# Optimization experiments

Measured on AMD Instinct MI355X. Metric: run time of the kernel, lower is better.

## Reference

```python
import jax, jax.numpy as jnp
import numpy as np

B, N, C_IN, C_CH = 1, 512, 128, 128

def layer_norm(x, g, b, eps=1e-5):
    mu = jnp.mean(x, axis=-1, keepdims=True)
    var = jnp.var(x, axis=-1, keepdims=True)
    return (x - mu) * jax.lax.rsqrt(var + eps) * g + b

def setup_inputs() -> dict:
    key = jax.random.key(0)
    ks = jax.random.split(key, 16)
    s = 0.02
    # weights stored as [in, out] (torch Linear uses y = x @ W.T + b; we pre-transpose)
    return {
        "z": jax.random.normal(ks[0], (B, N, N, C_IN), jnp.float32),
        "mask": jax.random.randint(ks[1], (B, N, N), 0, 2).astype(bool),
        "g_in": jnp.ones((C_IN,), jnp.float32),
        "b_in": jnp.zeros((C_IN,), jnp.float32),
        "Wa": jax.random.normal(ks[2], (C_IN, C_CH), jnp.float32) * s,
        "ba": jnp.zeros((C_CH,), jnp.float32),
        "Wga": jax.random.normal(ks[3], (C_IN, C_CH), jnp.float32) * s,
        "bga": jax.random.normal(ks[4], (C_CH,), jnp.float32) * s,
        "Wb": jax.random.normal(ks[5], (C_IN, C_CH), jnp.float32) * s,
        "bb": jnp.zeros((C_CH,), jnp.float32),
        "Wgb": jax.random.normal(ks[6], (C_IN, C_CH), jnp.float32) * s,
        "bgb": jax.random.normal(ks[7], (C_CH,), jnp.float32) * s,
        "g_o": jnp.ones((C_CH,), jnp.float32),
        "b_o": jnp.zeros((C_CH,), jnp.float32),
        "Wgo": jax.random.normal(ks[8], (C_IN, C_IN), jnp.float32) * s,
        "bgo": jax.random.normal(ks[9], (C_IN,), jnp.float32) * s,
        "Wo": jax.random.normal(ks[10], (C_CH, C_IN), jnp.float32) * s,
        "bo": jnp.zeros((C_IN,), jnp.float32),
    }

def reference(z, mask, g_in, b_in, Wa, ba, Wga, bga, Wb, bb, Wgb, bgb,
              g_o, b_o, Wgo, bgo, Wo, bo):
    zn = layer_norm(z, g_in, b_in)                                  # [B,N,N,Cin]
    a = jax.nn.sigmoid(zn @ Wga + bga) * (zn @ Wa + ba)             # [B,N,N,Cch]
    b = jax.nn.sigmoid(zn @ Wgb + bgb) * (zn @ Wb + bb)
    m = mask[..., None]                                             # [B,N,N,1]
    a = jnp.where(m, 0.0, a)
    b = jnp.where(m, 0.0, b)
    # axis == 1: k[b,i,j,o] = sum_k a[b,i,k,o] * b[b,j,k,o]
    k = jnp.einsum('biko,bjko->bijo', a, b)
    return jax.nn.sigmoid(zn @ Wgo + bgo) * (layer_norm(k, g_o, b_o) @ Wo + bo)
```

## Files before the change

### kernel.cpp

```cpp
#include <hip/hip_runtime.h>

#define NDIM 512
#define CDIM 128
#define RDIM (NDIM * NDIM)

typedef __attribute__((ext_vector_type(8))) short bf16x8;
typedef __attribute__((ext_vector_type(8))) unsigned short ushort8;
typedef __attribute__((ext_vector_type(4))) float f32x4;

__device__ __forceinline__ float bf2f(unsigned short u) {
  union { unsigned int i; float f; } v; v.i = ((unsigned int)u) << 16; return v.f;
}
__device__ __forceinline__ unsigned short f2bf(float f) {
  union { float f; unsigned int i; } v; v.f = f;
  unsigned int r = v.i + 0x7fffu + ((v.i >> 16) & 1u);
  return (unsigned short)(r >> 16);
}
__device__ __forceinline__ float sigm(float x) { return 1.0f / (1.0f + __expf(-x)); }

__device__ __forceinline__ int sw(int row, int col) {
  return (row << 7) + ((((col >> 3) ^ (row & 7)) << 3) | (col & 7));
}

__global__ __launch_bounds__(256) void k0_prep(
    const float* __restrict__ Wga, const float* __restrict__ Wa,
    const float* __restrict__ Wgb, const float* __restrict__ Wb,
    const float* __restrict__ Wgo, const float* __restrict__ Wo,
    unsigned short* __restrict__ wsW) {
  __shared__ unsigned short T[128 * 130];
  const float* src;
  switch (blockIdx.x) {
    case 0: src = Wga; break;
    case 1: src = Wa;  break;
    case 2: src = Wgb; break;
    case 3: src = Wb;  break;
    case 4: src = Wgo; break;
    default: src = Wo; break;
  }
  unsigned short* dst = wsW + blockIdx.x * (CDIM * CDIM);
  const int t = threadIdx.x;
  const int r = t >> 1, hf = t & 1;
  const float* s = src + r * CDIM + hf * 64;
  for (int i = 0; i < 64; i++) T[r * 130 + hf * 64 + i] = f2bf(s[i]);
  __syncthreads();
  unsigned short* d = dst + r * CDIM + hf * 64;
  for (int i = 0; i < 64; i++) d[i] = T[(hf * 64 + i) * 130 + r];
}

__global__ __launch_bounds__(256) void k1_proj(
    const float* __restrict__ z, const int* __restrict__ mask,
    const float* __restrict__ g_in, const float* __restrict__ b_in,
    const float* __restrict__ bga, const float* __restrict__ ba,
    const float* __restrict__ bgb, const float* __restrict__ bb,
    const float* __restrict__ bgo, const unsigned short* __restrict__ wsW,
    unsigned short* __restrict__ a_t, unsigned short* __restrict__ b_t,
    float* __restrict__ gate_out) {
  __shared__ unsigned short Xs[CDIM * CDIM];
  __shared__ unsigned short WT[CDIM * CDIM];
  const int t = threadIdx.x;
  const int lane = t & 63;
  const int w = t >> 6;
  const int l15 = lane & 15;
  const int lq = lane >> 4;
  const int row0 = blockIdx.x * 128;

  {
    const int row = t >> 1, hf = t & 1;
    const float4* zp = (const float4*)(z + (size_t)(row0 + row) * CDIM + hf * 64);
    float4 v[16];
    float s = 0.f, s2 = 0.f;
#pragma unroll
    for (int i = 0; i < 16; i++) {
      float4 x = zp[i];
      v[i] = x;
      s += x.x + x.y + x.z + x.w;
      s2 += x.x * x.x + x.y * x.y + x.z * x.z + x.w * x.w;
    }
    s += __shfl_xor(s, 1);
    s2 += __shfl_xor(s2, 1);
    const float mean = s * 0.0078125f;
    const float var = s2 * 0.0078125f - mean * mean;
    const float rs = rsqrtf(var + 1e-5f);
    const float4* gp = (const float4*)(g_in + hf * 64);
    const float4* bp = (const float4*)(b_in + hf * 64);
#pragma unroll
    for (int u = 0; u < 8; u++) {
      float4 x0 = v[2 * u], x1 = v[2 * u + 1];
      float4 g0 = gp[2 * u], g1 = gp[2 * u + 1];
      float4 c0 = bp[2 * u], c1 = bp[2 * u + 1];
      ushort8 pk;
      pk[0] = f2bf((x0.x - mean) * rs * g0.x + c0.x);
      pk[1] = f2bf((x0.y - mean) * rs * g0.y + c0.y);
      pk[2] = f2bf((x0.z - mean) * rs * g0.z + c0.z);
      pk[3] = f2bf((x0.w - mean) * rs * g0.w + c0.w);
      pk[4] = f2bf((x1.x - mean) * rs * g1.x + c1.x);
      pk[5] = f2bf((x1.y - mean) * rs * g1.y + c1.y);
      pk[6] = f2bf((x1.z - mean) * rs * g1.z + c1.z);
      pk[7] = f2bf((x1.w - mean) * rs * g1.w + c1.w);
      const int su = (hf * 8 + u) ^ (row & 7);
      *((ushort8*)&Xs[(row << 7) + (su << 3)]) = pk;
    }
  }

  unsigned mbits = 0;
#pragma unroll
  for (int ms = 0; ms < 2; ms++)
#pragma unroll
    for (int r = 0; r < 4; r++) {
      const int rl = w * 32 + ms * 16 + (lq << 2) + r;
      if (mask[row0 + rl] != 0) mbits |= 1u << (ms * 4 + r);
    }

  __syncthreads();

  bf16x8 afr[2][4];
#pragma unroll
  for (int ms = 0; ms < 2; ms++) {
    const int m = w * 32 + ms * 16 + l15;
#pragma unroll
    for (int kc = 0; kc < 4; kc++)
      afr[ms][kc] = *((const bf16x8*)&Xs[sw(m, kc * 32 + (lq << 3))]);
  }

  auto stageW = [&](int slot) {
    const unsigned short* Wg = wsW + slot * (CDIM * CDIM);
    const int o = t >> 1, hf = t & 1;
    const uint4* src = (const uint4*)(Wg + o * CDIM + hf * 64);
#pragma unroll
    for (int u = 0; u < 8; u++) {
      const int su = (hf * 8 + u) ^ (o & 7);
      *((uint4*)&WT[(o << 7) + (su << 3)]) = src[u];
    }
  };

  f32x4 accg[2][8], accv[2][8];
  const f32x4 zv = {0.f, 0.f, 0.f, 0.f};

  auto domfma = [&](f32x4 (&acc)[2][8]) {
#pragma unroll
    for (int kc = 0; kc < 4; kc++) {
      const int kk = kc * 32 + (lq << 3);
#pragma unroll
      for (int nf = 0; nf < 8; nf++) {
        bf16x8 bfr = *((const bf16x8*)&WT[sw(nf * 16 + l15, kk)]);
        acc[0][nf] = __builtin_amdgcn_mfma_f32_16x16x32_bf16(afr[0][kc], bfr, acc[0][nf], 0, 0, 0);
        acc[1][nf] = __builtin_amdgcn_mfma_f32_16x16x32_bf16(afr[1][kc], bfr, acc[1][nf], 0, 0, 0);
      }
    }
  };

#pragma unroll 1
  for (int pair = 0; pair < 2; pair++) {
#pragma unroll
    for (int i = 0; i < 2; i++)
#pragma unroll
      for (int j = 0; j < 8; j++) { accg[i][j] = zv; accv[i][j] = zv; }
    __syncthreads();
    stageW(pair * 2);
    __syncthreads();
    domfma(accg);
    __syncthreads();
    stageW(pair * 2 + 1);
    __syncthreads();
    domfma(accv);
    const float* bgp = (pair == 0) ? bga : bgb;
    const float* bvp = (pair == 0) ? ba : bb;
    __syncthreads();
#pragma unroll
    for (int ms = 0; ms < 2; ms++)
#pragma unroll
      for (int nf = 0; nf < 8; nf++) {
        const int n = nf * 16 + l15;
        const float bg = bgp[n], bv = bvp[n];
#pragma unroll
        for (int r = 0; r < 4; r++) {
          const int rl = w * 32 + ms * 16 + (lq << 2) + r;
          float val = sigm(accg[ms][nf][r] + bg) * (accv[ms][nf][r] + bv);
          if ((mbits >> (ms * 4 + r)) & 1u) val = 0.f;
          WT[sw(n, rl)] = f2bf(val);
        }
      }
    __syncthreads();
    unsigned short* dst = (pair == 0) ? a_t : b_t;
    {
      const int o = t >> 1, hf = t & 1;
#pragma unroll
      for (int u = 0; u < 8; u++) {
        const int ru = hf * 8 + u;
        const int su = ru ^ (o & 7);
        uint4 val = *((const uint4*)&WT[(o << 7) + (su << 3)]);
        *((uint4*)&dst[(size_t)o * RDIM + row0 + ru * 8]) = val;
      }
    }
  }

#pragma unroll
  for (int i = 0; i < 2; i++)
#pragma unroll
    for (int j = 0; j < 8; j++) accg[i][j] = zv;
  __syncthreads();
  stageW(4);
  __syncthreads();
  domfma(accg);
#pragma unroll
  for (int ms = 0; ms < 2; ms++)
#pragma unroll
    for (int nf = 0; nf < 8; nf++) {
      const int n = nf * 16 + l15;
      const float bg = bgo[n];
#pragma unroll
      for (int r = 0; r < 4; r++) {
        const int rl = w * 32 + ms * 16 + (lq << 2) + r;
        gate_out[(size_t)(row0 + rl) * CDIM + n] = sigm(accg[ms][nf][r] + bg);
      }
    }
}

__global__ __launch_bounds__(256) void k2_einsum(
    const unsigned short* __restrict__ a_t, const unsigned short* __restrict__ b_t,
    unsigned short* __restrict__ k_t) {
  __shared__ unsigned short As[128 * 72];
  __shared__ unsigned short Bs[128 * 72];
  const int t = threadIdx.x;
  const int lane = t & 63;
  const int w = t >> 6;
  const int l15 = lane & 15, lq = lane >> 4;
  const int o = blockIdx.x >> 4;
  const int tile = blockIdx.x & 15;
  const int i0 = (tile >> 2) * 128, j0 = (tile & 3) * 128;
  const size_t base = (size_t)o * RDIM;

  f32x4 acc[2][8];
  const f32x4 zv = {0.f, 0.f, 0.f, 0.f};
#pragma unroll
  for (int i = 0; i < 2; i++)
#pragma unroll
    for (int j = 0; j < 8; j++) acc[i][j] = zv;

  const int r = t & 127;
  const int isB = t >> 7;
  const unsigned short* srcp = (isB ? b_t : a_t) + base + (size_t)((isB ? j0 : i0) + r) * NDIM;
  unsigned short* dstp = isB ? &Bs[r * 72] : &As[r * 72];

  for (int k0 = 0; k0 < NDIM; k0 += 64) {
    __syncthreads();
    const uint4* s4 = (const uint4*)(srcp + k0);
#pragma unroll
    for (int u = 0; u < 8; u++) *((uint4*)&dstp[u * 8]) = s4[u];
    __syncthreads();
#pragma unroll
    for (int kc = 0; kc < 2; kc++) {
      const int kk = kc * 32 + (lq << 3);
      bf16x8 a0 = *((const bf16x8*)&As[(w * 32 + l15) * 72 + kk]);
      bf16x8 a1 = *((const bf16x8*)&As[(w * 32 + 16 + l15) * 72 + kk]);
#pragma unroll
      for (int nf = 0; nf < 8; nf++) {
        bf16x8 bfr = *((const bf16x8*)&Bs[(nf * 16 + l15) * 72 + kk]);
        acc[0][nf] = __builtin_amdgcn_mfma_f32_16x16x32_bf16(a0, bfr, acc[0][nf], 0, 0, 0);
        acc[1][nf] = __builtin_amdgcn_mfma_f32_16x16x32_bf16(a1, bfr, acc[1][nf], 0, 0, 0);
      }
    }
  }
#pragma unroll
  for (int ms = 0; ms < 2; ms++)
#pragma unroll
    for (int nf = 0; nf < 8; nf++)
#pragma unroll
      for (int r2 = 0; r2 < 4; r2++) {
        const int mi = i0 + w * 32 + ms * 16 + (lq << 2) + r2;
        const int nj = j0 + nf * 16 + l15;
        k_t[base + (size_t)mi * NDIM + nj] = f2bf(acc[ms][nf][r2]);
      }
}

__global__ __launch_bounds__(256) void k3_final(
    const unsigned short* __restrict__ k_t, const unsigned short* __restrict__ wsW,
    const float* __restrict__ g_o, const float* __restrict__ b_o,
    const float* __restrict__ bo, float* __restrict__ out) {
  __shared__ unsigned short Ks[CDIM * CDIM];
  __shared__ unsigned short XN[CDIM * CDIM];
  const int t = threadIdx.x;
  const int lane = t & 63;
  const int w = t >> 6;
  const int l15 = lane & 15, lq = lane >> 4;
  const int row0 = blockIdx.x * 128;

  {
    const int o = t >> 1, hf = t & 1;
    const uint4* src = (const uint4*)(k_t + (size_t)o * RDIM + row0 + hf * 64);
#pragma unroll
    for (int u = 0; u < 8; u++) {
      const int ru = hf * 8 + u;
      const int su = ru ^ (o & 7);
      *((uint4*)&Ks[(o << 7) + (su << 3)]) = src[u];
    }
  }
  __syncthreads();
  {
    const int row = t >> 1, hf = t & 1;
    float x[64];
    float s = 0.f, s2 = 0.f;
#pragma unroll
    for (int i = 0; i < 64; i++) {
      x[i] = bf2f(Ks[sw(hf * 64 + i, row)]);
      s += x[i];
      s2 += x[i] * x[i];
    }
    s += __shfl_xor(s, 1);
    s2 += __shfl_xor(s2, 1);
    const float mean = s * 0.0078125f;
    const float var = s2 * 0.0078125f - mean * mean;
    const float rs = rsqrtf(var + 1e-5f);
#pragma unroll
    for (int i = 0; i < 64; i++) {
      const int o = hf * 64 + i;
      XN[sw(row, o)] = f2bf((x[i] - mean) * rs * g_o[o] + b_o[o]);
    }
  }
  __syncthreads();
  {
    const unsigned short* Wg = wsW + 5 * (CDIM * CDIM);
    const int o = t >> 1, hf = t & 1;
    const uint4* src = (const uint4*)(Wg + o * CDIM + hf * 64);
#pragma unroll
    for (int u = 0; u < 8; u++) {
      const int su = (hf * 8 + u) ^ (o & 7);
      *((uint4*)&Ks[(o << 7) + (su << 3)]) = src[u];
    }
  }
  __syncthreads();

  f32x4 acc[2][8];
  const f32x4 zv = {0.f, 0.f, 0.f, 0.f};
#pragma unroll
  for (int i = 0; i < 2; i++)
#pragma unroll
    for (int j = 0; j < 8; j++) acc[i][j] = zv;

  bf16x8 afr[2][4];
#pragma unroll
  for (int ms = 0; ms < 2; ms++) {
    const int m = w * 32 + ms * 16 + l15;
#pragma unroll
    for (int kc = 0; kc < 4; kc++)
      afr[ms][kc] = *((const bf16x8*)&XN[sw(m, kc * 32 + (lq << 3))]);
  }
#pragma unroll
  for (int kc = 0; kc < 4; kc++) {
    const int kk = kc * 32 + (lq << 3);
#pragma unroll
    for (int nf = 0; nf < 8; nf++) {
      bf16x8 bfr = *((const bf16x8*)&Ks[sw(nf * 16 + l15, kk)]);
      acc[0][nf] = __builtin_amdgcn_mfma_f32_16x16x32_bf16(afr[0][kc], bfr, acc[0][nf], 0, 0, 0);
      acc[1][nf] = __builtin_amdgcn_mfma_f32_16x16x32_bf16(afr[1][kc], bfr, acc[1][nf], 0, 0, 0);
    }
  }
#pragma unroll
  for (int ms = 0; ms < 2; ms++)
#pragma unroll
    for (int nf = 0; nf < 8; nf++) {
      const int n = nf * 16 + l15;
      const float bn = bo[n];
#pragma unroll
      for (int r = 0; r < 4; r++) {
        const int rl = w * 32 + ms * 16 + (lq << 2) + r;
        const size_t idx = (size_t)(row0 + rl) * CDIM + n;
        out[idx] = out[idx] * (acc[ms][nf][r] + bn);
      }
    }
}

extern "C" void kernel_launch(void* const* d_in, const int* in_sizes, int n_in,
                              void* d_out, int out_size, void* d_ws, size_t ws_size,
                              hipStream_t stream) {
  const float* z    = (const float*)d_in[0];
  const int*   mask = (const int*)d_in[1];
  const float* g_in = (const float*)d_in[2];
  const float* b_in = (const float*)d_in[3];
  const float* Wa   = (const float*)d_in[4];
  const float* ba   = (const float*)d_in[5];
  const float* Wga  = (const float*)d_in[6];
  const float* bga  = (const float*)d_in[7];
  const float* Wb   = (const float*)d_in[8];
  const float* bb   = (const float*)d_in[9];
  const float* Wgb  = (const float*)d_in[10];
  const float* bgb  = (const float*)d_in[11];
  const float* g_o  = (const float*)d_in[12];
  const float* b_o  = (const float*)d_in[13];
  const float* Wgo  = (const float*)d_in[14];
  const float* bgo  = (const float*)d_in[15];
  const float* Wo   = (const float*)d_in[16];
  const float* bo   = (const float*)d_in[17];
  float* out = (float*)d_out;

  unsigned short* wsW = (unsigned short*)d_ws;
  unsigned short* a_t = wsW + 6 * (CDIM * CDIM);
  unsigned short* b_t = a_t + (size_t)CDIM * RDIM;
  unsigned short* k_t = b_t + (size_t)CDIM * RDIM;

  k0_prep<<<6, 256, 0, stream>>>(Wga, Wa, Wgb, Wb, Wgo, Wo, wsW);
  k1_proj<<<RDIM / 128, 256, 0, stream>>>(z, mask, g_in, b_in, bga, ba, bgb, bb,
                                          bgo, wsW, a_t, b_t, out);
  k2_einsum<<<CDIM * 16, 256, 0, stream>>>(a_t, b_t, k_t);
  k3_final<<<RDIM / 128, 256, 0, stream>>>(k_t, wsW, g_o, b_o, bo, out);
}
```

Measured before the change: 701.4 us.

## Prepack weights into MFMA fragment layout and drop LDS weight staging in projection

The prep kernel now also writes each weight matrix pre-arranged in per-lane MFMA B-fragment order, so the projection kernel loads weight fragments straight from global memory instead of staging them through a second 32KB shared buffer with barriers. The projection kernel also splits the output columns into two halves to shrink the accumulator register footprint, reloads z from global instead of holding it in registers, reuses the Xs buffer for the transposed output, and declares launch bounds requesting 3 blocks per CU. The aim is lower LDS use and register pressure for higher occupancy and fewer synchronisations, at the cost of more global/L2 traffic for weight fragments and a second read of z.

```diff
diff --git a/kernel.cpp b/kernel.cpp
--- a/kernel.cpp
+++ b/kernel.cpp
@@ -26,7 +26,7 @@
     const float* __restrict__ Wga, const float* __restrict__ Wa,
     const float* __restrict__ Wgb, const float* __restrict__ Wb,
     const float* __restrict__ Wgo, const float* __restrict__ Wo,
-    unsigned short* __restrict__ wsW) {
+    unsigned short* __restrict__ wsT, unsigned short* __restrict__ wsF) {
   __shared__ unsigned short T[128 * 130];
   const float* src;
   switch (blockIdx.x) {
@@ -37,42 +37,52 @@
     case 4: src = Wgo; break;
     default: src = Wo; break;
   }
-  unsigned short* dst = wsW + blockIdx.x * (CDIM * CDIM);
   const int t = threadIdx.x;
+  unsigned short* dstT = wsT + blockIdx.x * (CDIM * CDIM);
   const int r = t >> 1, hf = t & 1;
   const float* s = src + r * CDIM + hf * 64;
   for (int i = 0; i < 64; i++) T[r * 130 + hf * 64 + i] = f2bf(s[i]);
   __syncthreads();
-  unsigned short* d = dst + r * CDIM + hf * 64;
+  unsigned short* d = dstT + r * CDIM + hf * 64;
   for (int i = 0; i < 64; i++) d[i] = T[(hf * 64 + i) * 130 + r];
-}
-
-__global__ __launch_bounds__(256) void k1_proj(
+  unsigned short* dstF = wsF + blockIdx.x * 16384;
+  for (int gid = t; gid < 2048; gid += 256) {
+    const int fragid = gid >> 6, lane = gid & 63;
+    const int kc = fragid >> 3, nf = fragid & 7;
+    const int o = nf * 16 + (lane & 15);
+    const int c0 = kc * 32 + (lane >> 4) * 8;
+#pragma unroll
+    for (int j = 0; j < 8; j++) dstF[gid * 8 + j] = f2bf(src[(c0 + j) * CDIM + o]);
+  }
+}
+
+__device__ __forceinline__ bf16x8 ldfrag(const unsigned short* wf, int slot, int kc,
+                                         int nf, int lane) {
+  return *((const bf16x8*)(wf + (((slot * 32 + kc * 8 + nf) * 64 + lane) << 3)));
+}
+
+__global__ __launch_bounds__(256, 3) void k1_proj(
     const float* __restrict__ z, const int* __restrict__ mask,
     const float* __restrict__ g_in, const float* __restrict__ b_in,
     const float* __restrict__ bga, const float* __restrict__ ba,
     const float* __restrict__ bgb, const float* __restrict__ bb,
-    const float* __restrict__ bgo, const unsigned short* __restrict__ wsW,
+    const float* __restrict__ bgo, const unsigned short* __restrict__ wf,
     unsigned short* __restrict__ a_t, unsigned short* __restrict__ b_t,
     float* __restrict__ gate_out) {
   __shared__ unsigned short Xs[CDIM * CDIM];
-  __shared__ unsigned short WT[CDIM * CDIM];
   const int t = threadIdx.x;
   const int lane = t & 63;
   const int w = t >> 6;
-  const int l15 = lane & 15;
-  const int lq = lane >> 4;
+  const int l15 = lane & 15, lq = lane >> 4;
   const int row0 = blockIdx.x * 128;
 
   {
     const int row = t >> 1, hf = t & 1;
     const float4* zp = (const float4*)(z + (size_t)(row0 + row) * CDIM + hf * 64);
-    float4 v[16];
     float s = 0.f, s2 = 0.f;
 #pragma unroll
     for (int i = 0; i < 16; i++) {
       float4 x = zp[i];
-      v[i] = x;
       s += x.x + x.y + x.z + x.w;
       s2 += x.x * x.x + x.y * x.y + x.z * x.z + x.w * x.w;
     }
@@ -83,9 +93,9 @@
     const float rs = rsqrtf(var + 1e-5f);
     const float4* gp = (const float4*)(g_in + hf * 64);
     const float4* bp = (const float4*)(b_in + hf * 64);
-#pragma unroll
+#pragma unroll 4
     for (int u = 0; u < 8; u++) {
-      float4 x0 = v[2 * u], x1 = v[2 * u + 1];
+      float4 x0 = zp[2 * u], x1 = zp[2 * u + 1];
       float4 g0 = gp[2 * u], g1 = gp[2 * u + 1];
       float4 c0 = bp[2 * u], c1 = bp[2 * u + 1];
       ushort8 pk;
@@ -121,65 +131,50 @@
     for (int kc = 0; kc < 4; kc++)
       afr[ms][kc] = *((const bf16x8*)&Xs[sw(m, kc * 32 + (lq << 3))]);
   }
-
-  auto stageW = [&](int slot) {
-    const unsigned short* Wg = wsW + slot * (CDIM * CDIM);
-    const int o = t >> 1, hf = t & 1;
-    const uint4* src = (const uint4*)(Wg + o * CDIM + hf * 64);
-#pragma unroll
-    for (int u = 0; u < 8; u++) {
-      const int su = (hf * 8 + u) ^ (o & 7);
-      *((uint4*)&WT[(o << 7) + (su << 3)]) = src[u];
-    }
-  };
-
-  f32x4 accg[2][8], accv[2][8];
+  __syncthreads();
+
   const f32x4 zv = {0.f, 0.f, 0.f, 0.f};
-
-  auto domfma = [&](f32x4 (&acc)[2][8]) {
-#pragma unroll
-    for (int kc = 0; kc < 4; kc++) {
-      const int kk = kc * 32 + (lq << 3);
-#pragma unroll
-      for (int nf = 0; nf < 8; nf++) {
-        bf16x8 bfr = *((const bf16x8*)&WT[sw(nf * 16 + l15, kk)]);
-        acc[0][nf] = __builtin_amdgcn_mfma_f32_16x16x32_bf16(afr[0][kc], bfr, acc[0][nf], 0, 0, 0);
-        acc[1][nf] = __builtin_amdgcn_mfma_f32_16x16x32_bf16(afr[1][kc], bfr, acc[1][nf], 0, 0, 0);
-      }
-    }
-  };
 
 #pragma unroll 1
   for (int pair = 0; pair < 2; pair++) {
-#pragma unroll
-    for (int i = 0; i < 2; i++)
-#pragma unroll
-      for (int j = 0; j < 8; j++) { accg[i][j] = zv; accv[i][j] = zv; }
-    __syncthreads();
-    stageW(pair * 2);
-    __syncthreads();
-    domfma(accg);
-    __syncthreads();
-    stageW(pair * 2 + 1);
-    __syncthreads();
-    domfma(accv);
+    const int sg = pair * 2, sv = pair * 2 + 1;
     const float* bgp = (pair == 0) ? bga : bgb;
     const float* bvp = (pair == 0) ? ba : bb;
-    __syncthreads();
-#pragma unroll
-    for (int ms = 0; ms < 2; ms++)
-#pragma unroll
-      for (int nf = 0; nf < 8; nf++) {
-        const int n = nf * 16 + l15;
-        const float bg = bgp[n], bv = bvp[n];
-#pragma unroll
-        for (int r = 0; r < 4; r++) {
-          const int rl = w * 32 + ms * 16 + (lq << 2) + r;
-          float val = sigm(accg[ms][nf][r] + bg) * (accv[ms][nf][r] + bv);
-          if ((mbits >> (ms * 4 + r)) & 1u) val = 0.f;
-          WT[sw(n, rl)] = f2bf(val);
+#pragma unroll 1
+    for (int half = 0; half < 2; half++) {
+      f32x4 accg[2][4], accv[2][4];
+#pragma unroll
+      for (int i = 0; i < 2; i++)
+#pragma unroll
+        for (int j = 0; j < 4; j++) { accg[i][j] = zv; accv[i][j] = zv; }
+#pragma unroll
+      for (int kc = 0; kc < 4; kc++) {
+#pragma unroll
+        for (int nfh = 0; nfh < 4; nfh++) {
+          const int fi = half * 4 + nfh;
+          bf16x8 bg = ldfrag(wf, sg, kc, fi, lane);
+          bf16x8 bv = ldfrag(wf, sv, kc, fi, lane);
+          accg[0][nfh] = __builtin_amdgcn_mfma_f32_16x16x32_bf16(afr[0][kc], bg, accg[0][nfh], 0, 0, 0);
+          accg[1][nfh] = __builtin_amdgcn_mfma_f32_16x16x32_bf16(afr[1][kc], bg, accg[1][nfh], 0, 0, 0);
+          accv[0][nfh] = __builtin_amdgcn_mfma_f32_16x16x32_bf16(afr[0][kc], bv, accv[0][nfh], 0, 0, 0);
+          accv[1][nfh] = __builtin_amdgcn_mfma_f32_16x16x32_bf16(afr[1][kc], bv, accv[1][nfh], 0, 0, 0);
         }
       }
+#pragma unroll
+      for (int ms = 0; ms < 2; ms++)
+#pragma unroll
+        for (int nfh = 0; nfh < 4; nfh++) {
+          const int n = half * 64 + nfh * 16 + l15;
+          const float bg = bgp[n], bv = bvp[n];
+#pragma unroll
+          for (int r = 0; r < 4; r++) {
+            const int rl = w * 32 + ms * 16 + (lq << 2) + r;
+            float val = sigm(accg[ms][nfh][r] + bg) * (accv[ms][nfh][r] + bv);
+            if ((mbits >> (ms * 4 + r)) & 1u) val = 0.f;
+            Xs[sw(n, rl)] = f2bf(val);
+          }
+        }
+    }
     __syncthreads();
     unsigned short* dst = (pair == 0) ? a_t : b_t;
     {
@@ -188,32 +183,42 @@
       for (int u = 0; u < 8; u++) {
         const int ru = hf * 8 + u;
         const int su = ru ^ (o & 7);
-        uint4 val = *((const uint4*)&WT[(o << 7) + (su << 3)]);
+        uint4 val = *((const uint4*)&Xs[(o << 7) + (su << 3)]);
         *((uint4*)&dst[(size_t)o * RDIM + row0 + ru * 8]) = val;
       }
     }
-  }
-
-#pragma unroll
-  for (int i = 0; i < 2; i++)
-#pragma unroll
-    for (int j = 0; j < 8; j++) accg[i][j] = zv;
-  __syncthreads();
-  stageW(4);
-  __syncthreads();
-  domfma(accg);
-#pragma unroll
-  for (int ms = 0; ms < 2; ms++)
-#pragma unroll
-    for (int nf = 0; nf < 8; nf++) {
-      const int n = nf * 16 + l15;
-      const float bg = bgo[n];
-#pragma unroll
-      for (int r = 0; r < 4; r++) {
-        const int rl = w * 32 + ms * 16 + (lq << 2) + r;
-        gate_out[(size_t)(row0 + rl) * CDIM + n] = sigm(accg[ms][nf][r] + bg);
-      }
-    }
+    __syncthreads();
+  }
+
+#pragma unroll 1
+  for (int half = 0; half < 2; half++) {
+    f32x4 accg[2][4];
+#pragma unroll
+    for (int i = 0; i < 2; i++)
+#pragma unroll
+      for (int j = 0; j < 4; j++) accg[i][j] = zv;
+#pragma unroll
+    for (int kc = 0; kc < 4; kc++) {
+#pragma unroll
+      for (int nfh = 0; nfh < 4; nfh++) {
+        bf16x8 bg = ldfrag(wf, 4, kc, half * 4 + nfh, lane);
+        accg[0][nfh] = __builtin_amdgcn_mfma_f32_16x16x32_bf16(afr[0][kc], bg, accg[0][nfh], 0, 0, 0);
+        accg[1][nfh] = __builtin_amdgcn_mfma_f32_16x16x32_bf16(afr[1][kc], bg, accg[1][nfh], 0, 0, 0);
+      }
+    }
+#pragma unroll
+    for (int ms = 0; ms < 2; ms++)
+#pragma unroll
+      for (int nfh = 0; nfh < 4; nfh++) {
+        const int n = half * 64 + nfh * 16 + l15;
+        const float bg = bgo[n];
+#pragma unroll
+        for (int r = 0; r < 4; r++) {
+          const int rl = w * 32 + ms * 16 + (lq << 2) + r;
+          gate_out[(size_t)(row0 + rl) * CDIM + n] = sigm(accg[ms][nfh][r] + bg);
+        }
+      }
+  }
 }
 
 __global__ __launch_bounds__(256) void k2_einsum(
@@ -393,14 +398,15 @@
   const float* bo   = (const float*)d_in[17];
   float* out = (float*)d_out;
 
-  unsigned short* wsW = (unsigned short*)d_ws;
-  unsigned short* a_t = wsW + 6 * (CDIM * CDIM);
+  unsigned short* wsT = (unsigned short*)d_ws;
+  unsigned short* wsF = wsT + 6 * (CDIM * CDIM);
+  unsigned short* a_t = wsF + 6 * (CDIM * CDIM);
   unsigned short* b_t = a_t + (size_t)CDIM * RDIM;
   unsigned short* k_t = b_t + (size_t)CDIM * RDIM;
 
-  k0_prep<<<6, 256, 0, stream>>>(Wga, Wa, Wgb, Wb, Wgo, Wo, wsW);
+  k0_prep<<<6, 256, 0, stream>>>(Wga, Wa, Wgb, Wb, Wgo, Wo, wsT, wsF);
   k1_proj<<<RDIM / 128, 256, 0, stream>>>(z, mask, g_in, b_in, bga, ba, bgb, bb,
-                                          bgo, wsW, a_t, b_t, out);
+                                          bgo, wsF, a_t, b_t, out);
   k2_einsum<<<CDIM * 16, 256, 0, stream>>>(a_t, b_t, k_t);
-  k3_final<<<RDIM / 128, 256, 0, stream>>>(k_t, wsW, g_o, b_o, bo, out);
-}
+  k3_final<<<RDIM / 128, 256, 0, stream>>>(k_t, wsT, g_o, b_o, bo, out);
+}
```

Result: faster. 674.1 us (-3.9%).
